# Kernel optimization log

Hardware: AMD Instinct MI355X
Metric: run time of the kernel (lower is better)

The kernel has to match this reference:

```python
import jax, jax.numpy as jnp
import numpy as np

N_NODES = 262144
N_EDGES = 524288
N_GRAPHS = 8192
BN_EPS = 1e-5


def setup_inputs() -> dict:
    key = jax.random.key(0)
    ks = jax.random.split(key, 12)
    x = jax.random.normal(ks[0], (N_NODES, 77), dtype=jnp.float32)
    edge_index = jax.random.randint(ks[1], (2, N_EDGES), 0, N_NODES, dtype=jnp.int32)
    # sorted segment ids covering every graph (arange-style fill)
    batch = (jnp.arange(N_NODES, dtype=jnp.int32) * N_GRAPHS // N_NODES).astype(jnp.int32)
    s77 = 1.0 / np.sqrt(77.0)
    s128 = 1.0 / np.sqrt(128.0)
    return {
        "x": x,
        "edge_index": edge_index,
        "batch": batch,
        "w0a": jax.random.normal(ks[2], (77, 128), dtype=jnp.float32) * s77,
        "b0a": jnp.zeros((128,), jnp.float32),
        "w0b": jax.random.normal(ks[3], (128, 128), dtype=jnp.float32) * s128,
        "b0b": jnp.zeros((128,), jnp.float32),
        "wa": jax.random.normal(ks[4], (4, 128, 128), dtype=jnp.float32) * s128,
        "ba": jnp.zeros((4, 128), jnp.float32),
        "wb": jax.random.normal(ks[5], (4, 128, 128), dtype=jnp.float32) * s128,
        "bb": jnp.zeros((4, 128), jnp.float32),
        "gamma": jnp.ones((5, 128), jnp.float32),
        "beta": jnp.zeros((5, 128), jnp.float32),
    }


def _gin_encoder(x, edge_index, batch, w0a, b0a, w0b, b0b, wa, ba, wb, bb, gamma, beta):
    n = x.shape[0]
    src, dst = edge_index[0], edge_index[1]
    h = x
    pooled = []
    for i in range(5):
        # GINConv (eps=0): agg_i = h_i + sum_{(j,i) in E} h_j, then 2-layer MLP
        agg = h + jax.ops.segment_sum(h[src], dst, num_segments=n)
        if i == 0:
            w1, c1, w2, c2 = w0a, b0a, w0b, b0b
        else:
            w1, c1, w2, c2 = wa[i - 1], ba[i - 1], wb[i - 1], bb[i - 1]
        h = jax.nn.relu(agg @ w1 + c1) @ w2 + c2
        h = jax.nn.relu(h)
        # BatchNorm1d (training-mode batch statistics, biased variance)
        mean = jnp.mean(h, axis=0)
        var = jnp.mean(jnp.square(h - mean), axis=0)
        h = gamma[i] * (h - mean) * jax.lax.rsqrt(var + BN_EPS) + beta[i]
        pooled.append(jax.ops.segment_max(h, batch, num_segments=N_GRAPHS))
    return jnp.concatenate(pooled, axis=1)  # [N_GRAPHS, 640]


def reference(x, edge_index, batch, w0a, b0a, w0b, b0b, wa, ba, wb, bb, gamma, beta):
    return _gin_encoder(x, edge_index, batch, w0a, b0a, w0b, b0b, wa, ba, wb, bb, gamma, beta)
```

## Files before the change

### kernel.cpp

```cpp
#include <hip/hip_runtime.h>
#include <cstdint>
#include <cstddef>

#define N_NODES_C 262144
#define N_EDGES_C 524288
#define N_GRAPHS_C 8192
#define BN_EPS_C 1e-5f

typedef short short8 __attribute__((ext_vector_type(8)));
typedef float f32x4 __attribute__((ext_vector_type(4)));

union Frag { int2 p2[2]; short8 v8; };

__device__ __forceinline__ unsigned short f2bf(float f) {
  unsigned int u = __float_as_uint(f);
  u += 0x7fffu + ((u >> 16) & 1u);
  return (unsigned short)(u >> 16);
}
__device__ __forceinline__ float bf2f(unsigned short h) {
  return __uint_as_float(((unsigned int)h) << 16);
}

__global__ __launch_bounds__(256) void hist_kernel(const int* __restrict__ dst, int* __restrict__ cnt) {
  int e = blockIdx.x * 256 + threadIdx.x;
  if (e < N_EDGES_C) atomicAdd(&cnt[dst[e]], 1);
}

__global__ __launch_bounds__(256) void scanA_kernel(const int* __restrict__ cnt,
                                                    int* __restrict__ rs, int* __restrict__ bsums) {
  __shared__ int lds[256];
  const int b = blockIdx.x, t = threadIdx.x;
  int4 v = ((const int4*)(cnt + b * 1024))[t];
  lds[t] = v.x + v.y + v.z + v.w;
  __syncthreads();
  for (int off = 1; off < 256; off <<= 1) {
    int add = (t >= off) ? lds[t - off] : 0;
    __syncthreads();
    lds[t] += add;
    __syncthreads();
  }
  int excl = (t > 0) ? lds[t - 1] : 0;
  if (t == 255) bsums[b] = lds[255];
  int4 o;
  o.x = excl; o.y = excl + v.x; o.z = excl + v.x + v.y; o.w = excl + v.x + v.y + v.z;
  ((int4*)(rs + b * 1024))[t] = o;
}

__global__ __launch_bounds__(256) void scanB_kernel(int* __restrict__ bsums) {
  __shared__ int lds[256];
  const int t = threadIdx.x;
  lds[t] = bsums[t];
  __syncthreads();
  for (int off = 1; off < 256; off <<= 1) {
    int add = (t >= off) ? lds[t - off] : 0;
    __syncthreads();
    lds[t] += add;
    __syncthreads();
  }
  bsums[t] = (t > 0) ? lds[t - 1] : 0;
}

__global__ __launch_bounds__(256) void scanC_kernel(int* __restrict__ rs, int* __restrict__ cursor,
                                                    const int* __restrict__ bsums) {
  int i = blockIdx.x * 256 + threadIdx.x;
  int v = rs[i] + bsums[i >> 10];
  rs[i] = v;
  cursor[i] = v;
  if (i == 0) rs[N_NODES_C] = N_EDGES_C;
}

__global__ __launch_bounds__(256) void edge_bucket_kernel(const int* __restrict__ src,
                                                          const int* __restrict__ dst,
                                                          int* __restrict__ cursor,
                                                          int* __restrict__ ebuf) {
  int e = blockIdx.x * 256 + threadIdx.x;
  if (e >= N_EDGES_C) return;
  int pos = atomicAdd(&cursor[dst[e]], 1);
  ebuf[pos] = src[e];
}

__global__ __launch_bounds__(256) void agg77_kernel(const float* __restrict__ x,
                                                    const int* __restrict__ rs,
                                                    const int* __restrict__ ebuf,
                                                    float* __restrict__ agg) {
  int idx = blockIdx.x * 256 + threadIdx.x;
  int n = idx >> 5, q = idx & 31;
  int s = rs[n], e = rs[n + 1];
  const size_t nb = (size_t)n * 77;
  float v0 = x[nb + q];
  float v1 = x[nb + q + 32];
  float v2 = (q < 13) ? x[nb + q + 64] : 0.f;
  for (int i = s; i < e; ++i) {
    const size_t sb = (size_t)ebuf[i] * 77;
    v0 += x[sb + q];
    v1 += x[sb + q + 32];
    if (q < 13) v2 += x[sb + q + 64];
  }
  const size_t ob = (size_t)n * 128;
  agg[ob + q] = v0;
  agg[ob + q + 32] = v1;
  agg[ob + q + 64] = (q < 13) ? v2 : 0.f;
  agg[ob + q + 96] = 0.f;
}

__global__ __launch_bounds__(256) void wsplit_kernel(const float* __restrict__ w0a,
                                                     const float* __restrict__ w0b,
                                                     const float* __restrict__ wa,
                                                     const float* __restrict__ wb,
                                                     unsigned short* __restrict__ Wpk) {
  int tid = blockIdx.x * 256 + threadIdx.x;
  int m = tid >> 11;
  int rem = tid & 2047;
  int f = rem >> 6;
  int l = rem & 63;
  int ct = f >> 2, ks = f & 3;
  int c = ct * 16 + (l & 15);
  const size_t mb = (size_t)m * 32768;
  const size_t fl = (size_t)(f * 64 + l) * 4;
#pragma unroll
  for (int j = 0; j < 8; ++j) {
    int k = ks * 32 + ((l >> 4) << 3) + j;
    float w;
    if (m == 0)      w = (k < 77) ? w0a[k * 128 + c] : 0.f;
    else if (m == 1) w = w0b[k * 128 + c];
    else if (m < 6)  w = wa[(size_t)(m - 2) * 16384 + k * 128 + c];
    else             w = wb[(size_t)(m - 6) * 16384 + k * 128 + c];
    unsigned short hh = f2bf(w);
    unsigned short ll = f2bf(w - bf2f(hh));
    if (j < 4) {
      Wpk[mb + fl + j] = hh;
      Wpk[mb + 16384 + fl + j] = ll;
    } else {
      Wpk[mb + 8192 + fl + (j - 4)] = hh;
      Wpk[mb + 24576 + fl + (j - 4)] = ll;
    }
  }
}

template <bool GATHER>
__global__ __launch_bounds__(512, 2) void fused_layer_kernel(
    const float* __restrict__ Hin,
    const int* __restrict__ rs,
    const int* __restrict__ ebuf,
    const float* __restrict__ Sprev,
    const float* __restrict__ gprev,
    const float* __restrict__ bprev,
    const unsigned short* __restrict__ W1pk,
    const unsigned short* __restrict__ W2pk,
    const float* __restrict__ b1,
    const float* __restrict__ b2,
    float* __restrict__ Hout,
    float* __restrict__ Sout) {
  __shared__ int4 sW2[4096];
  __shared__ int4 sW1C[4096];
  __shared__ float bsum[128];
  __shared__ float bsq[128];

  const int t = threadIdx.x;
  const int lane = t & 63;
  const int wv = t >> 6;
  const int cb = lane & 15;
  const int g = lane >> 4;

  {
    const int4* s2 = (const int4*)W2pk;
#pragma unroll
    for (int i = 0; i < 8; ++i) sW2[t + i * 512] = s2[t + i * 512];
  }

  float bc1[8], bc2[8];
#pragma unroll
  for (int ct = 0; ct < 8; ++ct) {
    bc1[ct] = b1[ct * 16 + cb];
    bc2[ct] = b2[ct * 16 + cb];
  }

  f32x4 scv[8], shv[8];
  if constexpr (GATHER) {
    const float inv_n = 1.0f / (float)N_NODES_C;
#pragma unroll
    for (int q = 0; q < 8; ++q) {
      int f0 = (q >> 1) * 32 + g * 8 + (q & 1) * 4;
#pragma unroll
      for (int j = 0; j < 4; ++j) {
        int f = f0 + j;
        float mean = Sprev[f] * inv_n;
        float var = Sprev[128 + f] * inv_n - mean * mean;
        float sc = gprev[f] * rsqrtf(var + BN_EPS_C);
        scv[q][j] = sc;
        shv[q][j] = bprev[f] - mean * sc;
      }
    }
  }

  float ssum[8] = {}, ssq[8] = {};
  const size_t blockRow0 = (size_t)blockIdx.x * 1024;

  for (int it = 0; it < 8; ++it) {
    const size_t strip = blockRow0 + it * 128;
    const size_t wrow0 = strip + wv * 16;

    __syncthreads();
    {
      const int4* s1 = (const int4*)W1pk;
#pragma unroll
      for (int i = 0; i < 8; ++i) sW1C[t + i * 512] = s1[t + i * 512];
    }

    f32x4 va[8];
    {
      const size_t r = wrow0 + cb;
      const float* hp = Hin + r * 128 + g * 8;
#pragma unroll
      for (int q = 0; q < 8; ++q)
        va[q] = *(const f32x4*)(hp + (q >> 1) * 32 + (q & 1) * 4);
      if constexpr (GATHER) {
        int s = rs[r], e = rs[r + 1];
        for (int i = s; i < e; ++i) {
          const float* hq = Hin + (size_t)ebuf[i] * 128 + g * 8;
#pragma unroll
          for (int q = 0; q < 8; ++q)
            va[q] += *(const f32x4*)(hq + (q >> 1) * 32 + (q & 1) * 4);
        }
        float cnt = (float)(e - s + 1);
#pragma unroll
        for (int q = 0; q < 8; ++q) va[q] = va[q] * scv[q] + cnt * shv[q];
      }
    }

    Frag ah[4], al[4];
#pragma unroll
    for (int ks = 0; ks < 4; ++ks) {
#pragma unroll
      for (int j = 0; j < 8; ++j) {
        float fv = va[ks * 2 + (j >> 2)][j & 3];
        unsigned short hh = f2bf(fv);
        ah[ks].v8[j] = (short)hh;
        al[ks].v8[j] = (short)f2bf(fv - bf2f(hh));
      }
    }

    __syncthreads();

    f32x4 d1[8] = {};
    {
      const int2* R1 = (const int2*)sW1C;
#pragma unroll
      for (int ks = 0; ks < 4; ++ks) {
#pragma unroll
        for (int ct = 0; ct < 8; ++ct) {
          int fi = (ct * 4 + ks) * 64 + lane;
          Frag wh, wl;
          wh.p2[0] = R1[fi];        wh.p2[1] = R1[2048 + fi];
          wl.p2[0] = R1[4096 + fi]; wl.p2[1] = R1[6144 + fi];
          d1[ct] = __builtin_amdgcn_mfma_f32_16x16x32_bf16(ah[ks].v8, wh.v8, d1[ct], 0, 0, 0);
          d1[ct] = __builtin_amdgcn_mfma_f32_16x16x32_bf16(al[ks].v8, wh.v8, d1[ct], 0, 0, 0);
          d1[ct] = __builtin_amdgcn_mfma_f32_16x16x32_bf16(ah[ks].v8, wl.v8, d1[ct], 0, 0, 0);
        }
      }
    }
    __syncthreads();

    {
      char* c1b = (char*)sW1C;
#pragma unroll
      for (int ct = 0; ct < 8; ++ct) {
#pragma unroll
        for (int j = 0; j < 4; ++j) {
          int r = wv * 16 + g * 4 + j;
          int c = ct * 16 + cb;
          float v = fmaxf(d1[ct][j] + bc1[ct], 0.f);
          *(float*)(c1b + ((r * 512 + c * 4) ^ ((r & 7) << 4))) = v;
        }
      }
    }
    __syncthreads();

    f32x4 d2[8] = {};
    {
      const int rr = wv * 16 + cb;
      const char* c1r = (const char*)sW1C;
      const int2* R2 = (const int2*)sW2;
#pragma unroll
      for (int ks = 0; ks < 4; ++ks) {
        int base = rr * 512 + ks * 128 + g * 32;
        f32x4 x0 = *(const f32x4*)(c1r + ((base) ^ ((rr & 7) << 4)));
        f32x4 x1 = *(const f32x4*)(c1r + ((base + 16) ^ ((rr & 7) << 4)));
        Frag a2h, a2l;
#pragma unroll
        for (int j = 0; j < 8; ++j) {
          float fv = (j < 4) ? x0[j] : x1[j - 4];
          unsigned short hh = f2bf(fv);
          a2h.v8[j] = (short)hh;
          a2l.v8[j] = (short)f2bf(fv - bf2f(hh));
        }
#pragma unroll
        for (int ct = 0; ct < 8; ++ct) {
          int fi = (ct * 4 + ks) * 64 + lane;
          Frag wh, wl;
          wh.p2[0] = R2[fi];        wh.p2[1] = R2[2048 + fi];
          wl.p2[0] = R2[4096 + fi]; wl.p2[1] = R2[6144 + fi];
          d2[ct] = __builtin_amdgcn_mfma_f32_16x16x32_bf16(a2h.v8, wh.v8, d2[ct], 0, 0, 0);
          d2[ct] = __builtin_amdgcn_mfma_f32_16x16x32_bf16(a2l.v8, wh.v8, d2[ct], 0, 0, 0);
          d2[ct] = __builtin_amdgcn_mfma_f32_16x16x32_bf16(a2h.v8, wl.v8, d2[ct], 0, 0, 0);
        }
      }
    }

#pragma unroll
    for (int ct = 0; ct < 8; ++ct) {
      const int c = ct * 16 + cb;
#pragma unroll
      for (int j = 0; j < 4; ++j) {
        size_t r = wrow0 + g * 4 + j;
        float v = fmaxf(d2[ct][j] + bc2[ct], 0.f);
        Hout[r * 128 + c] = v;
        ssum[ct] += v;
        ssq[ct] += v * v;
      }
    }
  }

  if (t < 128) { bsum[t] = 0.f; bsq[t] = 0.f; }
  __syncthreads();
#pragma unroll
  for (int ct = 0; ct < 8; ++ct) {
    atomicAdd(&bsum[ct * 16 + cb], ssum[ct]);
    atomicAdd(&bsq[ct * 16 + cb], ssq[ct]);
  }
  __syncthreads();
  if (t < 128) {
    atomicAdd(&Sout[t], bsum[t]);
    atomicAdd(&Sout[128 + t], bsq[t]);
  }
}

__global__ __launch_bounds__(256) void pool_kernel(const float* __restrict__ h,
                                                   const float* __restrict__ stats,
                                                   const float* __restrict__ gamma,
                                                   const float* __restrict__ beta,
                                                   float* __restrict__ out, int layer) {
  __shared__ float red[256];
  const int gph = blockIdx.x;
  const int t = threadIdx.x;
  const int f = t & 127, half = t >> 7;

  const float inv_n = 1.0f / (float)N_NODES_C;
  float mean = stats[f] * inv_n;
  float var = stats[128 + f] * inv_n - mean * mean;
  float sc = gamma[f] * rsqrtf(var + BN_EPS_C);
  float sh = beta[f] - mean * sc;

  float m = -3.4e38f;
  size_t base = ((size_t)gph * 32 + half * 16) * 128 + f;
#pragma unroll
  for (int r = 0; r < 16; ++r)
    m = fmaxf(m, h[base + (size_t)r * 128] * sc + sh);
  red[t] = m;
  __syncthreads();
  if (t < 128) out[(size_t)gph * 640 + layer * 128 + f] = fmaxf(red[t], red[t + 128]);
}

extern "C" void kernel_launch(void* const* d_in, const int* in_sizes, int n_in,
                              void* d_out, int out_size, void* d_ws, size_t ws_size,
                              hipStream_t stream) {
  const float* x = (const float*)d_in[0];
  const int* ei = (const int*)d_in[1];
  const int* src = ei;
  const int* dst = ei + N_EDGES_C;
  const float* w0a = (const float*)d_in[3];
  const float* b0a = (const float*)d_in[4];
  const float* w0b = (const float*)d_in[5];
  const float* b0b = (const float*)d_in[6];
  const float* wa = (const float*)d_in[7];
  const float* ba = (const float*)d_in[8];
  const float* wb = (const float*)d_in[9];
  const float* bb = (const float*)d_in[10];
  const float* gamma = (const float*)d_in[11];
  const float* beta = (const float*)d_in[12];
  float* out = (float*)d_out;

  const size_t NNf = (size_t)N_NODES_C * 128;
  float* ws = (float*)d_ws;
  float* Hb0 = ws;
  float* Hb1 = ws + NNf;
  float* STATS = ws + 2 * NNf;
  int* cnt = (int*)(STATS + 5 * 256);
  int* rowstart = cnt + N_NODES_C;
  int* cursor = rowstart + N_NODES_C + 4;
  int* bsums = cursor + N_NODES_C;
  int* ebuf = bsums + 256;
  unsigned short* Wpk = (unsigned short*)(((uintptr_t)(ebuf + N_EDGES_C) + 63) & ~(uintptr_t)63);

  wsplit_kernel<<<80, 256, 0, stream>>>(w0a, w0b, wa, wb, Wpk);
  hipMemsetAsync(cnt, 0, N_NODES_C * sizeof(int), stream);
  hipMemsetAsync(STATS, 0, 5 * 256 * sizeof(float), stream);
  hist_kernel<<<N_EDGES_C / 256, 256, 0, stream>>>(dst, cnt);
  scanA_kernel<<<256, 256, 0, stream>>>(cnt, rowstart, bsums);
  scanB_kernel<<<1, 256, 0, stream>>>(bsums);
  scanC_kernel<<<N_NODES_C / 256, 256, 0, stream>>>(rowstart, cursor, bsums);
  edge_bucket_kernel<<<N_EDGES_C / 256, 256, 0, stream>>>(src, dst, cursor, ebuf);

  agg77_kernel<<<(N_NODES_C * 32) / 256, 256, 0, stream>>>(x, rowstart, ebuf, Hb1);
  fused_layer_kernel<false><<<256, 512, 0, stream>>>(
      Hb1, rowstart, ebuf, nullptr, nullptr, nullptr,
      Wpk + 0 * 32768, Wpk + 1 * 32768, b0a, b0b, Hb0, STATS + 0 * 256);
  pool_kernel<<<N_GRAPHS_C, 256, 0, stream>>>(Hb0, STATS + 0 * 256, gamma, beta, out, 0);

  float* cur = Hb0;
  float* nxt = Hb1;
  for (int i = 1; i < 5; ++i) {
    fused_layer_kernel<true><<<256, 512, 0, stream>>>(
        cur, rowstart, ebuf,
        STATS + (size_t)(i - 1) * 256, gamma + (size_t)(i - 1) * 128, beta + (size_t)(i - 1) * 128,
        Wpk + (size_t)(2 + (i - 1)) * 32768, Wpk + (size_t)(6 + (i - 1)) * 32768,
        ba + (size_t)(i - 1) * 128, bb + (size_t)(i - 1) * 128,
        nxt, STATS + (size_t)i * 256);
    pool_kernel<<<N_GRAPHS_C, 256, 0, stream>>>(nxt, STATS + (size_t)i * 256,
                                                gamma + (size_t)i * 128, beta + (size_t)i * 128,
                                                out, i);
    float* tmp = cur; cur = nxt; nxt = tmp;
  }
}
```

Baseline: 1.706 ms.

## Split gather out of MLP kernel and fuse per-graph max/min pooling into MLP

Moves the neighbor gather plus BatchNorm affine out of the MLP kernel into a separate coalesced float4 aggregation kernel. The MLP kernel now runs in place, prefetches the next strip's rows during the current strip's work, and computes per-graph column max and min in its epilogue. Pooling then applies the BN affine to those reductions, picking max or min by the sign of the scale, instead of re-reading the full H. This adds an extra pass over H for aggregation and extra barriers, but removes the gather-induced latency stalls inside the MFMA kernel and the pool kernel's full-tensor read.

```diff
diff --git a/kernel.cpp b/kernel.cpp
--- a/kernel.cpp
+++ b/kernel.cpp
@@ -103,6 +103,40 @@
   agg[ob + q + 96] = 0.f;
 }
 
+__global__ __launch_bounds__(256) void aggbn_kernel(const float4* __restrict__ h4,
+                                                    const int* __restrict__ rs,
+                                                    const int* __restrict__ ebuf,
+                                                    const float* __restrict__ S,
+                                                    const float* __restrict__ gamma,
+                                                    const float* __restrict__ beta,
+                                                    float4* __restrict__ out4) {
+  int idx = blockIdx.x * 256 + threadIdx.x;
+  int n = idx >> 5, q = idx & 31;
+  const float inv_n = 1.0f / (float)N_NODES_C;
+  float sc[4], sh[4];
+#pragma unroll
+  for (int j = 0; j < 4; ++j) {
+    int f = q * 4 + j;
+    float mean = S[f] * inv_n;
+    float var = S[128 + f] * inv_n - mean * mean;
+    float s = gamma[f] * rsqrtf(var + BN_EPS_C);
+    sc[j] = s;
+    sh[j] = beta[f] - mean * s;
+  }
+  int s0 = rs[n], e0 = rs[n + 1];
+  float4 v = h4[(size_t)n * 32 + q];
+  for (int i = s0; i < e0; ++i) {
+    float4 u = h4[(size_t)ebuf[i] * 32 + q];
+    v.x += u.x; v.y += u.y; v.z += u.z; v.w += u.w;
+  }
+  float cnt = (float)(e0 - s0 + 1);
+  v.x = v.x * sc[0] + cnt * sh[0];
+  v.y = v.y * sc[1] + cnt * sh[1];
+  v.z = v.z * sc[2] + cnt * sh[2];
+  v.w = v.w * sc[3] + cnt * sh[3];
+  out4[(size_t)n * 32 + q] = v;
+}
+
 __global__ __launch_bounds__(256) void wsplit_kernel(const float* __restrict__ w0a,
                                                      const float* __restrict__ w0b,
                                                      const float* __restrict__ wa,
@@ -137,22 +171,18 @@
   }
 }
 
-template <bool GATHER>
-__global__ __launch_bounds__(512, 2) void fused_layer_kernel(
-    const float* __restrict__ Hin,
-    const int* __restrict__ rs,
-    const int* __restrict__ ebuf,
-    const float* __restrict__ Sprev,
-    const float* __restrict__ gprev,
-    const float* __restrict__ bprev,
-    const unsigned short* __restrict__ W1pk,
-    const unsigned short* __restrict__ W2pk,
-    const float* __restrict__ b1,
-    const float* __restrict__ b2,
-    float* __restrict__ Hout,
-    float* __restrict__ Sout) {
+__global__ __launch_bounds__(512, 2) void mlp_kernel(float* __restrict__ H,
+                                                     const unsigned short* __restrict__ W1pk,
+                                                     const unsigned short* __restrict__ W2pk,
+                                                     const float* __restrict__ b1,
+                                                     const float* __restrict__ b2,
+                                                     float* __restrict__ Sout,
+                                                     float* __restrict__ gmax,
+                                                     float* __restrict__ gmin) {
   __shared__ int4 sW2[4096];
   __shared__ int4 sW1C[4096];
+  __shared__ float gmM[8][128];
+  __shared__ float gmN[8][128];
   __shared__ float bsum[128];
   __shared__ float bsq[128];
 
@@ -175,26 +205,16 @@
     bc2[ct] = b2[ct * 16 + cb];
   }
 
-  f32x4 scv[8], shv[8];
-  if constexpr (GATHER) {
-    const float inv_n = 1.0f / (float)N_NODES_C;
-#pragma unroll
-    for (int q = 0; q < 8; ++q) {
-      int f0 = (q >> 1) * 32 + g * 8 + (q & 1) * 4;
-#pragma unroll
-      for (int j = 0; j < 4; ++j) {
-        int f = f0 + j;
-        float mean = Sprev[f] * inv_n;
-        float var = Sprev[128 + f] * inv_n - mean * mean;
-        float sc = gprev[f] * rsqrtf(var + BN_EPS_C);
-        scv[q][j] = sc;
-        shv[q][j] = bprev[f] - mean * sc;
-      }
-    }
-  }
-
   float ssum[8] = {}, ssq[8] = {};
   const size_t blockRow0 = (size_t)blockIdx.x * 1024;
+
+  f32x4 va[8];
+  {
+    const float* hp = H + (blockRow0 + wv * 16 + cb) * 128 + g * 8;
+#pragma unroll
+    for (int q = 0; q < 8; ++q)
+      va[q] = *(const f32x4*)(hp + (q >> 1) * 32 + (q & 1) * 4);
+  }
 
   for (int it = 0; it < 8; ++it) {
     const size_t strip = blockRow0 + it * 128;
@@ -205,27 +225,6 @@
       const int4* s1 = (const int4*)W1pk;
 #pragma unroll
       for (int i = 0; i < 8; ++i) sW1C[t + i * 512] = s1[t + i * 512];
-    }
-
-    f32x4 va[8];
-    {
-      const size_t r = wrow0 + cb;
-      const float* hp = Hin + r * 128 + g * 8;
-#pragma unroll
-      for (int q = 0; q < 8; ++q)
-        va[q] = *(const f32x4*)(hp + (q >> 1) * 32 + (q & 1) * 4);
-      if constexpr (GATHER) {
-        int s = rs[r], e = rs[r + 1];
-        for (int i = s; i < e; ++i) {
-          const float* hq = Hin + (size_t)ebuf[i] * 128 + g * 8;
-#pragma unroll
-          for (int q = 0; q < 8; ++q)
-            va[q] += *(const f32x4*)(hq + (q >> 1) * 32 + (q & 1) * 4);
-        }
-        float cnt = (float)(e - s + 1);
-#pragma unroll
-        for (int q = 0; q < 8; ++q) va[q] = va[q] * scv[q] + cnt * shv[q];
-      }
     }
 
     Frag ah[4], al[4];
@@ -261,6 +260,13 @@
     }
     __syncthreads();
 
+    if (it < 7) {
+      const float* hp = H + (blockRow0 + (it + 1) * 128 + wv * 16 + cb) * 128 + g * 8;
+#pragma unroll
+      for (int q = 0; q < 8; ++q)
+        va[q] = *(const f32x4*)(hp + (q >> 1) * 32 + (q & 1) * 4);
+    }
+
     {
       char* c1b = (char*)sW1C;
 #pragma unroll
@@ -310,14 +316,31 @@
 #pragma unroll
     for (int ct = 0; ct < 8; ++ct) {
       const int c = ct * 16 + cb;
+      float mx = 0.f;
+      float mn = 3.4e38f;
 #pragma unroll
       for (int j = 0; j < 4; ++j) {
         size_t r = wrow0 + g * 4 + j;
         float v = fmaxf(d2[ct][j] + bc2[ct], 0.f);
-        Hout[r * 128 + c] = v;
+        H[r * 128 + c] = v;
         ssum[ct] += v;
         ssq[ct] += v * v;
+        mx = fmaxf(mx, v);
+        mn = fminf(mn, v);
       }
+      mx = fmaxf(mx, __shfl_xor(mx, 16));
+      mx = fmaxf(mx, __shfl_xor(mx, 32));
+      mn = fminf(mn, __shfl_xor(mn, 16));
+      mn = fminf(mn, __shfl_xor(mn, 32));
+      if (lane < 16) { gmM[wv][c] = mx; gmN[wv][c] = mn; }
+    }
+    __syncthreads();
+
+    {
+      int gl = t >> 7, f = t & 127;
+      size_t gg = (strip >> 5) + gl;
+      gmax[gg * 128 + f] = fmaxf(gmM[2 * gl][f], gmM[2 * gl + 1][f]);
+      gmin[gg * 128 + f] = fminf(gmN[2 * gl][f], gmN[2 * gl + 1][f]);
     }
   }
 
@@ -335,30 +358,21 @@
   }
 }
 
-__global__ __launch_bounds__(256) void pool_kernel(const float* __restrict__ h,
+__global__ __launch_bounds__(256) void pool_kernel(const float* __restrict__ gmax,
+                                                   const float* __restrict__ gmin,
                                                    const float* __restrict__ stats,
                                                    const float* __restrict__ gamma,
                                                    const float* __restrict__ beta,
                                                    float* __restrict__ out, int layer) {
-  __shared__ float red[256];
-  const int gph = blockIdx.x;
-  const int t = threadIdx.x;
-  const int f = t & 127, half = t >> 7;
-
+  int id = blockIdx.x * 256 + threadIdx.x;
+  int gg = id >> 7, f = id & 127;
   const float inv_n = 1.0f / (float)N_NODES_C;
   float mean = stats[f] * inv_n;
   float var = stats[128 + f] * inv_n - mean * mean;
   float sc = gamma[f] * rsqrtf(var + BN_EPS_C);
   float sh = beta[f] - mean * sc;
-
-  float m = -3.4e38f;
-  size_t base = ((size_t)gph * 32 + half * 16) * 128 + f;
-#pragma unroll
-  for (int r = 0; r < 16; ++r)
-    m = fmaxf(m, h[base + (size_t)r * 128] * sc + sh);
-  red[t] = m;
-  __syncthreads();
-  if (t < 128) out[(size_t)gph * 640 + layer * 128 + f] = fmaxf(red[t], red[t + 128]);
+  float v = (sc >= 0.f ? gmax[id] : gmin[id]) * sc + sh;
+  out[(size_t)gg * 640 + layer * 128 + f] = v;
 }
 
 extern "C" void kernel_launch(void* const* d_in, const int* in_sizes, int n_in,
@@ -385,7 +399,9 @@
   float* Hb0 = ws;
   float* Hb1 = ws + NNf;
   float* STATS = ws + 2 * NNf;
-  int* cnt = (int*)(STATS + 5 * 256);
+  float* gmax = STATS + 5 * 256;
+  float* gmin = gmax + (size_t)N_GRAPHS_C * 128;
+  int* cnt = (int*)(gmin + (size_t)N_GRAPHS_C * 128);
   int* rowstart = cnt + N_NODES_C;
   int* cursor = rowstart + N_NODES_C + 4;
   int* bsums = cursor + N_NODES_C;
@@ -401,24 +417,27 @@
   scanC_kernel<<<N_NODES_C / 256, 256, 0, stream>>>(rowstart, cursor, bsums);
   edge_bucket_kernel<<<N_EDGES_C / 256, 256, 0, stream>>>(src, dst, cursor, ebuf);
 
+  const int PB = (N_GRAPHS_C * 128) / 256;
+
   agg77_kernel<<<(N_NODES_C * 32) / 256, 256, 0, stream>>>(x, rowstart, ebuf, Hb1);
-  fused_layer_kernel<false><<<256, 512, 0, stream>>>(
-      Hb1, rowstart, ebuf, nullptr, nullptr, nullptr,
-      Wpk + 0 * 32768, Wpk + 1 * 32768, b0a, b0b, Hb0, STATS + 0 * 256);
-  pool_kernel<<<N_GRAPHS_C, 256, 0, stream>>>(Hb0, STATS + 0 * 256, gamma, beta, out, 0);
-
-  float* cur = Hb0;
-  float* nxt = Hb1;
+  mlp_kernel<<<256, 512, 0, stream>>>(Hb1, Wpk, Wpk + 32768, b0a, b0b,
+                                      STATS, gmax, gmin);
+  pool_kernel<<<PB, 256, 0, stream>>>(gmax, gmin, STATS, gamma, beta, out, 0);
+
+  float* cur = Hb1;
+  float* oth = Hb0;
   for (int i = 1; i < 5; ++i) {
-    fused_layer_kernel<true><<<256, 512, 0, stream>>>(
-        cur, rowstart, ebuf,
+    aggbn_kernel<<<(N_NODES_C * 32) / 256, 256, 0, stream>>>(
+        (const float4*)cur, rowstart, ebuf,
         STATS + (size_t)(i - 1) * 256, gamma + (size_t)(i - 1) * 128, beta + (size_t)(i - 1) * 128,
-        Wpk + (size_t)(2 + (i - 1)) * 32768, Wpk + (size_t)(6 + (i - 1)) * 32768,
-        ba + (size_t)(i - 1) * 128, bb + (size_t)(i - 1) * 128,
-        nxt, STATS + (size_t)i * 256);
-    pool_kernel<<<N_GRAPHS_C, 256, 0, stream>>>(nxt, STATS + (size_t)i * 256,
-                                                gamma + (size_t)i * 128, beta + (size_t)i * 128,
-                                                out, i);
-    float* tmp = cur; cur = nxt; nxt = tmp;
-  }
-}
+        (float4*)oth);
+    mlp_kernel<<<256, 512, 0, stream>>>(oth,
+                                        Wpk + (size_t)(1 + i) * 32768,
+                                        Wpk + (size_t)(5 + i) * 32768,
+                                        ba + (size_t)(i - 1) * 128, bb + (size_t)(i - 1) * 128,
+                                        STATS + (size_t)i * 256, gmax, gmin);
+    pool_kernel<<<PB, 256, 0, stream>>>(gmax, gmin, STATS + (size_t)i * 256,
+                                        gamma + (size_t)i * 128, beta + (size_t)i * 128, out, i);
+    float* tmp = cur; cur = oth; oth = tmp;
+  }
+}
```

Result: slower. 1.931 ms (+13.2%).
